# Performance work log

Measured on AMD Instinct MI355X. Metric: run time of the kernel, lower is better.

Reference implementation:

```python
import jax, jax.numpy as jnp
import numpy as np

SEGMENT_LENGTHS = [2048, 4096, 8192]
DILATION_RATES = [1, 2, 4]
EPS = 1e-8


def setup_inputs() -> dict:
    key = jax.random.key(0)
    kq, kk, kv = jax.random.split(key, 3)
    shape = (4, 8192, 8, 64)  # (b, n, h, d)
    return {
        "query": jax.random.normal(kq, shape, dtype=jnp.float32),
        "key": jax.random.normal(kk, shape, dtype=jnp.float32),
        "value": jax.random.normal(kv, shape, dtype=jnp.float32),
    }


def _dilated_attention(query, key, value):
    b, n, h, d = query.shape
    ng = len(SEGMENT_LENGTHS)
    group_sizes = [h // ng] * ng
    for i in range(h % ng):
        group_sizes[i] += 1
    scale = 1.0 / (d ** 0.5)  # torch SDPA default: 1/sqrt(E), E = last dim

    out = jnp.zeros_like(query)
    for i, (g, r, s) in enumerate(zip(group_sizes, DILATION_RATES, SEGMENT_LENGTHS)):
        offset = i % r
        hmin = sum(group_sizes[:i])
        hmax = hmin + g
        nseg = n // s
        # (b, nseg, s, h, d) -> strided dilation slice + head-group slice
        qg = query.reshape(b, nseg, s, h, d)[:, :, offset::r, hmin:hmax, :]
        kg = key.reshape(b, nseg, s, h, d)[:, :, offset::r, hmin:hmax, :]
        vg = value.reshape(b, nseg, s, h, d)[:, :, offset::r, hmin:hmax, :]
        # Faithful to the torch code: SDPA is fed (bn, s, h, d) untransposed, so
        # attention is over the HEAD axis (length g); s is a batch-like axis.
        scores = jnp.einsum('bnsqd,bnskd->bnsqk', qg, kg) * scale  # (b,nseg,sd,g,g)
        attn = jax.nn.softmax(scores, axis=-1)
        x = jnp.einsum('bnsqk,bnskd->bnsqd', attn, vg)  # (b,nseg,sd,g,d)
        # custom sum-normalization over (segment, dilated-position) dims
        x = x / (x.sum(axis=(1, 2), keepdims=True) + EPS)
        # scatter-add back into the strided/head-sliced locations
        out = (out.reshape(b, nseg, s, h, d)
                  .at[:, :, offset::r, hmin:hmax, :].add(x)
                  .reshape(b, n, h, d))
    return out / ng


def reference(query, key, value):
    return _dilated_attention(query, key, value)
```

## Files before the change

### kernel.cpp

```cpp
#include <hip/hip_runtime.h>
#include <math.h>

#define NB 4
#define NN 8192
#define NH 8
#define ND 64
#define NPART_STRIDE 192
#define N_BLOCKS_P1 1792
#define N_WAVES_P1  (N_BLOCKS_P1 * 4)


template<int G, int IT>
__device__ __forceinline__ void pass1_work(
    const float* __restrict__ Q, const float* __restrict__ K,
    const float* __restrict__ V, float* __restrict__ out,
    float* __restrict__ partials,
    int b, int chunk, int r, int off, int hmin, int seglen)
{
    const int tid  = threadIdx.x;
    const int w    = tid >> 6;
    const int lane = tid & 63;
    const int sg   = lane >> 4;
    const int l    = lane & 15;

    size_t rowbase[IT];
    #pragma unroll
    for (int it = 0; it < IT; ++it) {
        const int j   = chunk * (16 * IT) + w * (4 * IT) + it * 4 + sg;
        const int seg = j >> 11;
        const int td  = j & 2047;
        const int pos = seg * seglen + off + td * r;
        rowbase[it] = (((size_t)b * NN + pos) * NH + hmin) * ND + 4 * l;
    }

    float4 qv[IT][G], kv[IT][G], vv[IT][G];
    #pragma unroll
    for (int it = 0; it < IT; ++it)
        #pragma unroll
        for (int q = 0; q < G; ++q) {
            qv[it][q] = *(const float4*)(Q + rowbase[it] + q * ND);
            kv[it][q] = *(const float4*)(K + rowbase[it] + q * ND);
            vv[it][q] = *(const float4*)(V + rowbase[it] + q * ND);
        }

    float xs[G][4];
    #pragma unroll
    for (int q = 0; q < G; ++q)
        #pragma unroll
        for (int e = 0; e < 4; ++e) xs[q][e] = 0.f;

    #pragma unroll
    for (int it = 0; it < IT; ++it) {
        float sc[G][G];
        #pragma unroll
        for (int q = 0; q < G; ++q)
            #pragma unroll
            for (int k = 0; k < G; ++k)
                sc[q][k] = qv[it][q].x * kv[it][k].x + qv[it][q].y * kv[it][k].y
                         + qv[it][q].z * kv[it][k].z + qv[it][q].w * kv[it][k].w;

        #pragma unroll
        for (int o = 8; o >= 1; o >>= 1)
            #pragma unroll
            for (int q = 0; q < G; ++q)
                #pragma unroll
                for (int k = 0; k < G; ++k)
                    sc[q][k] += __shfl_xor(sc[q][k], o);

        #pragma unroll
        for (int q = 0; q < G; ++q) {
            float m = -INFINITY;
            #pragma unroll
            for (int k = 0; k < G; ++k) { sc[q][k] *= 0.125f; m = fmaxf(m, sc[q][k]); }
            float a[G]; float ssum = 0.f;
            #pragma unroll
            for (int k = 0; k < G; ++k) { a[k] = __expf(sc[q][k] - m); ssum += a[k]; }
            const float rs = 1.f / ssum;
            float xe0 = 0.f, xe1 = 0.f, xe2 = 0.f, xe3 = 0.f;
            #pragma unroll
            for (int k = 0; k < G; ++k) {
                const float aw = a[k] * rs;
                xe0 += aw * vv[it][k].x; xe1 += aw * vv[it][k].y;
                xe2 += aw * vv[it][k].z; xe3 += aw * vv[it][k].w;
            }
            *(float4*)(out + rowbase[it] + (size_t)q * ND) =
                make_float4(xe0, xe1, xe2, xe3);
            xs[q][0] += xe0; xs[q][1] += xe1; xs[q][2] += xe2; xs[q][3] += xe3;
        }
    }

    #pragma unroll
    for (int q = 0; q < G; ++q)
        #pragma unroll
        for (int e = 0; e < 4; ++e) {
            xs[q][e] += __shfl_xor(xs[q][e], 16);
            xs[q][e] += __shfl_xor(xs[q][e], 32);
        }

    if (lane < 16) {
        const int wid = blockIdx.x * 4 + w;
        #pragma unroll
        for (int q = 0; q < G; ++q)
            *(float4*)(partials + (size_t)wid * NPART_STRIDE + q * 64 + 4 * l) =
                make_float4(xs[q][0], xs[q][1], xs[q][2], xs[q][3]);
    }
}

__global__ __launch_bounds__(256)
void sda_pass1(const float* __restrict__ Q, const float* __restrict__ K,
               const float* __restrict__ V, float* __restrict__ out,
               float* __restrict__ partials)
{
    const int bid = blockIdx.x;
    if (bid < 1024) {
        const int b = bid >> 8, chunk = bid & 255;
        pass1_work<3, 2>(Q, K, V, out, partials, b, chunk, 1, 0, 0, 2048);
    } else if (bid < 1536) {
        const int loc = bid - 1024;
        const int b = loc >> 7, chunk = loc & 127;
        pass1_work<3, 2>(Q, K, V, out, partials, b, chunk, 2, 1, 3, 4096);
    } else {
        const int loc = bid - 1536;
        const int b = loc >> 6, chunk = loc & 63;
        pass1_work<2, 2>(Q, K, V, out, partials, b, chunk, 4, 2, 6, 8192);
    }
}

__global__ __launch_bounds__(256)
void sda_pass2a(const float* __restrict__ partials, float* __restrict__ partial2)
{
    const int bid   = blockIdx.x;
    const int bh    = bid >> 3;
    const int slice = bid & 7;
    const int b     = bh >> 3;
    const int h     = bh & 7;
    const int d     = threadIdx.x & 63;
    const int part  = threadIdx.x >> 6;
    int qi, wstart, cnt;
    if (h < 3)      { qi = h;     wstart = b * 1024;       cnt = 1024; }
    else if (h < 6) { qi = h - 3; wstart = 4096 + b * 512; cnt = 512;  }
    else            { qi = h - 6; wstart = 6144 + b * 256; cnt = 256;  }
    const int len = cnt >> 3;
    const int c0  = wstart + slice * len;
    float s = 0.f;
    #pragma unroll 4
    for (int c = part; c < len; c += 4)
        s += partials[(size_t)(c0 + c) * NPART_STRIDE + qi * 64 + d];
    __shared__ float sred[4][64];
    sred[part][d] = s;
    __syncthreads();
    if (part == 0)
        partial2[(size_t)bid * 64 + d] = sred[0][d] + sred[1][d] + sred[2][d] + sred[3][d];
}

__global__ __launch_bounds__(256)
void sda_pass2b(const float* __restrict__ partial2, float* __restrict__ inv)
{
    const int t = blockIdx.x * 256 + threadIdx.x;
    if (t >= NB * NH * ND) return;
    const int bh = t >> 6;
    const int d  = t & 63;
    float s = 0.f;
    #pragma unroll
    for (int sl = 0; sl < 8; ++sl)
        s += partial2[(size_t)(bh * 8 + sl) * 64 + d];
    inv[t] = 1.f / (3.f * (s + 1e-8f));
}

__global__ __launch_bounds__(256)
void sda_pass3(float* __restrict__ out, const float* __restrict__ inv)
{
    const int total4 = NB * NN * NH * ND / 4;
    for (int idx = blockIdx.x * 256 + threadIdx.x; idx < total4;
         idx += gridDim.x * 256) {
        const int d4  = idx & 15;
        const int rem = idx >> 4;
        const int h   = rem & 7;
        const int pos = (rem >> 3) & 8191;
        const int b   = rem >> 16;
        const bool cov = (h < 3) || ((h < 6) ? ((pos & 1) == 1) : ((pos & 3) == 2));
        float4 o;
        if (cov) {
            const float4 v = ((const float4*)out)[idx];
            const float4 f = ((const float4*)inv)[b * 128 + h * 16 + d4];
            o = make_float4(v.x * f.x, v.y * f.y, v.z * f.z, v.w * f.w);
        } else {
            o = make_float4(0.f, 0.f, 0.f, 0.f);
        }
        ((float4*)out)[idx] = o;
    }
}

extern "C" void kernel_launch(void* const* d_in, const int* in_sizes, int n_in,
                              void* d_out, int out_size, void* d_ws, size_t ws_size,
                              hipStream_t stream)
{
    const float* Q = (const float*)d_in[0];
    const float* K = (const float*)d_in[1];
    const float* V = (const float*)d_in[2];
    float* out      = (float*)d_out;
    float* partials = (float*)d_ws;
    float* partial2 = partials + (size_t)N_WAVES_P1 * NPART_STRIDE;
    float* inv      = partial2 + 256 * 64;

    hipLaunchKernelGGL(sda_pass1,  dim3(N_BLOCKS_P1), dim3(256), 0, stream,
                       Q, K, V, out, partials);
    hipLaunchKernelGGL(sda_pass2a, dim3(256), dim3(256), 0, stream, partials, partial2);
    hipLaunchKernelGGL(sda_pass2b, dim3(8),   dim3(256), 0, stream, partial2, inv);
    hipLaunchKernelGGL(sda_pass3,  dim3(2048), dim3(256), 0, stream, out, inv);
}
```

Before: 54.28 us.

## Stage unnormalized attention outputs as compact bf16 buffer in workspace

Pass 1 now writes its per-position attention output in bf16 to a dense, compacted workspace buffer instead of fp32 into the strided output tensor. Pass 3 reads the compact bf16 values, scales them by the normalization factor, and writes the final fp32 output including the zeros. This halves intermediate write/read traffic and avoids pass 3 reading the full output. The cost is bf16 rounding of intermediate values before normalization, which may break tolerance, and it relies on a large enough workspace.

```diff
diff --git a/kernel.cpp b/kernel.cpp
--- a/kernel.cpp
+++ b/kernel.cpp
@@ -1,5 +1,6 @@
 #include <hip/hip_runtime.h>
 #include <math.h>
+
 
 #define NB 4
 #define NN 8192
@@ -9,13 +10,25 @@
 #define N_BLOCKS_P1 1792
 #define N_WAVES_P1  (N_BLOCKS_P1 * 4)
 
+#define XBASE_G1 (32768u * 192u)
+#define XBASE_G2 (XBASE_G1 + 16384u * 192u)
+
+__device__ __forceinline__ unsigned short f2b(float f) {
+    unsigned int u = __float_as_uint(f);
+    u = (u + 0x7FFFu + ((u >> 16) & 1u)) >> 16;
+    return (unsigned short)u;
+}
+__device__ __forceinline__ float b2f(unsigned short s) {
+    return __uint_as_float(((unsigned int)s) << 16);
+}
 
 template<int G, int IT>
 __device__ __forceinline__ void pass1_work(
     const float* __restrict__ Q, const float* __restrict__ K,
-    const float* __restrict__ V, float* __restrict__ out,
+    const float* __restrict__ V, unsigned short* __restrict__ xc,
     float* __restrict__ partials,
-    int b, int chunk, int r, int off, int hmin, int seglen)
+    int b, int chunk, int r, int off, int hmin, int seglen,
+    size_t xbase, int ninst, int xrec)
 {
     const int tid  = threadIdx.x;
     const int w    = tid >> 6;
@@ -24,12 +37,12 @@
     const int l    = lane & 15;
 
     size_t rowbase[IT];
+    int jj[IT];
     #pragma unroll
     for (int it = 0; it < IT; ++it) {
         const int j   = chunk * (16 * IT) + w * (4 * IT) + it * 4 + sg;
-        const int seg = j >> 11;
-        const int td  = j & 2047;
-        const int pos = seg * seglen + off + td * r;
+        const int pos = (j >> 11) * seglen + off + (j & 2047) * r;
+        jj[it] = j;
         rowbase[it] = (((size_t)b * NN + pos) * NH + hmin) * ND + 4 * l;
     }
 
@@ -72,19 +85,27 @@
             float m = -INFINITY;
             #pragma unroll
             for (int k = 0; k < G; ++k) { sc[q][k] *= 0.125f; m = fmaxf(m, sc[q][k]); }
-            float a[G]; float ssum = 0.f;
-            #pragma unroll
-            for (int k = 0; k < G; ++k) { a[k] = __expf(sc[q][k] - m); ssum += a[k]; }
+            float ssum = 0.f;
+            #pragma unroll
+            for (int k = 0; k < G; ++k) { sc[q][k] = __expf(sc[q][k] - m); ssum += sc[q][k]; }
             const float rs = 1.f / ssum;
+            #pragma unroll
+            for (int k = 0; k < G; ++k) sc[q][k] *= rs;
+        }
+
+        const size_t xo0 = xbase + ((size_t)b * ninst + jj[it]) * xrec;
+        #pragma unroll
+        for (int q = 0; q < G; ++q) {
             float xe0 = 0.f, xe1 = 0.f, xe2 = 0.f, xe3 = 0.f;
             #pragma unroll
             for (int k = 0; k < G; ++k) {
-                const float aw = a[k] * rs;
+                const float aw = sc[q][k];
                 xe0 += aw * vv[it][k].x; xe1 += aw * vv[it][k].y;
                 xe2 += aw * vv[it][k].z; xe3 += aw * vv[it][k].w;
             }
-            *(float4*)(out + rowbase[it] + (size_t)q * ND) =
-                make_float4(xe0, xe1, xe2, xe3);
+            ushort4 u;
+            u.x = f2b(xe0); u.y = f2b(xe1); u.z = f2b(xe2); u.w = f2b(xe3);
+            *(ushort4*)(xc + xo0 + q * 64 + 4 * l) = u;
             xs[q][0] += xe0; xs[q][1] += xe1; xs[q][2] += xe2; xs[q][3] += xe3;
         }
     }
@@ -108,21 +129,24 @@
 
 __global__ __launch_bounds__(256)
 void sda_pass1(const float* __restrict__ Q, const float* __restrict__ K,
-               const float* __restrict__ V, float* __restrict__ out,
+               const float* __restrict__ V, unsigned short* __restrict__ xc,
                float* __restrict__ partials)
 {
     const int bid = blockIdx.x;
     if (bid < 1024) {
         const int b = bid >> 8, chunk = bid & 255;
-        pass1_work<3, 2>(Q, K, V, out, partials, b, chunk, 1, 0, 0, 2048);
+        pass1_work<3, 2>(Q, K, V, xc, partials, b, chunk, 1, 0, 0, 2048,
+                         0, 8192, 192);
     } else if (bid < 1536) {
         const int loc = bid - 1024;
         const int b = loc >> 7, chunk = loc & 127;
-        pass1_work<3, 2>(Q, K, V, out, partials, b, chunk, 2, 1, 3, 4096);
+        pass1_work<3, 2>(Q, K, V, xc, partials, b, chunk, 2, 1, 3, 4096,
+                         XBASE_G1, 4096, 192);
     } else {
         const int loc = bid - 1536;
         const int b = loc >> 6, chunk = loc & 63;
-        pass1_work<2, 2>(Q, K, V, out, partials, b, chunk, 4, 2, 6, 8192);
+        pass1_work<2, 2>(Q, K, V, xc, partials, b, chunk, 4, 2, 6, 8192,
+                         XBASE_G2, 2048, 128);
     }
 }
 
@@ -168,7 +192,8 @@
 }
 
 __global__ __launch_bounds__(256)
-void sda_pass3(float* __restrict__ out, const float* __restrict__ inv)
+void sda_pass3(const unsigned short* __restrict__ xc, float* __restrict__ out,
+               const float* __restrict__ inv)
 {
     const int total4 = NB * NN * NH * ND / 4;
     for (int idx = blockIdx.x * 256 + threadIdx.x; idx < total4;
@@ -178,14 +203,27 @@
         const int h   = rem & 7;
         const int pos = (rem >> 3) & 8191;
         const int b   = rem >> 16;
-        const bool cov = (h < 3) || ((h < 6) ? ((pos & 1) == 1) : ((pos & 3) == 2));
-        float4 o;
-        if (cov) {
-            const float4 v = ((const float4*)out)[idx];
-            const float4 f = ((const float4*)inv)[b * 128 + h * 16 + d4];
-            o = make_float4(v.x * f.x, v.y * f.y, v.z * f.z, v.w * f.w);
+
+        float4 o = make_float4(0.f, 0.f, 0.f, 0.f);
+        size_t xo = (size_t)-1;
+        if (h < 3) {
+            xo = ((size_t)b * 8192 + pos) * 192 + h * 64 + 4 * d4;
+        } else if (h < 6) {
+            if (pos & 1) {
+                const int j = (pos >> 12) * 2048 + ((pos & 4095) >> 1);
+                xo = XBASE_G1 + ((size_t)b * 4096 + j) * 192 + (h - 3) * 64 + 4 * d4;
+            }
         } else {
-            o = make_float4(0.f, 0.f, 0.f, 0.f);
+            if ((pos & 3) == 2) {
+                const int j = (pos - 2) >> 2;
+                xo = XBASE_G2 + ((size_t)b * 2048 + j) * 128 + (h - 6) * 64 + 4 * d4;
+            }
+        }
+        if (xo != (size_t)-1) {
+            const ushort4 u = *(const ushort4*)(xc + xo);
+            const float4 f = ((const float4*)inv)[(b * 8 + h) * 16 + d4];
+            o = make_float4(b2f(u.x) * f.x, b2f(u.y) * f.y,
+                            b2f(u.z) * f.z, b2f(u.w) * f.w);
         }
         ((float4*)out)[idx] = o;
     }
@@ -198,14 +236,16 @@
     const float* Q = (const float*)d_in[0];
     const float* K = (const float*)d_in[1];
     const float* V = (const float*)d_in[2];
-    float* out      = (float*)d_out;
-    float* partials = (float*)d_ws;
+    float* out = (float*)d_out;
+
+    unsigned short* xc = (unsigned short*)d_ws;
+    float* partials = (float*)((char*)d_ws + 22u * 1024u * 1024u);
     float* partial2 = partials + (size_t)N_WAVES_P1 * NPART_STRIDE;
     float* inv      = partial2 + 256 * 64;
 
     hipLaunchKernelGGL(sda_pass1,  dim3(N_BLOCKS_P1), dim3(256), 0, stream,
-                       Q, K, V, out, partials);
+                       Q, K, V, xc, partials);
     hipLaunchKernelGGL(sda_pass2a, dim3(256), dim3(256), 0, stream, partials, partial2);
     hipLaunchKernelGGL(sda_pass2b, dim3(8),   dim3(256), 0, stream, partial2, inv);
-    hipLaunchKernelGGL(sda_pass3,  dim3(2048), dim3(256), 0, stream, out, inv);
-}
+    hipLaunchKernelGGL(sda_pass3,  dim3(2048), dim3(256), 0, stream, xc, out, inv);
+}
```

After: 48.82 us. 1.11x faster.
